# Kernel tuning notes

Hardware: AMD Instinct MI355X
Metric: run time of the kernel (lower is better)

The kernel has to match this reference:

```python
import jax, jax.numpy as jnp
import numpy as np

NUM_USERS = 200000
NUM_ITEMS = 100000
N_NODES = NUM_USERS + NUM_ITEMS
EMB_DIM = 64
NUM_LAYERS = 3
N_EDGES = 4800000


def setup_inputs() -> dict:
    key = jax.random.key(0)
    k1, k2, k3, k4, k5 = jax.random.split(key, 5)
    # Xavier-uniform-ish init scale for embeddings
    bound = float(np.sqrt(6.0 / (N_NODES + EMB_DIM)))
    user_emb = jax.random.uniform(k1, (NUM_USERS, EMB_DIM), jnp.float32, -bound, bound)
    item_emb = jax.random.uniform(k2, (NUM_ITEMS, EMB_DIM), jnp.float32, -bound, bound)
    adj_rows = jax.random.randint(k3, (N_EDGES,), 0, N_NODES, jnp.int32)
    adj_cols = jax.random.randint(k4, (N_EDGES,), 0, N_NODES, jnp.int32)
    # stand-in for symmetric-normalized adjacency values
    adj_vals = jax.random.uniform(k5, (N_EDGES,), jnp.float32) / 16.0
    return {"user_emb": user_emb, "item_emb": item_emb,
            "adj_rows": adj_rows, "adj_cols": adj_cols, "adj_vals": adj_vals}


def _spmm(rows, cols, vals, x):
    # y[r] = sum_{e: rows[e]==r} vals[e] * x[cols[e]]  -- COO SpMM
    gathered = x[cols] * vals[:, None]          # [E, D]
    return jax.ops.segment_sum(gathered, rows, num_segments=N_NODES)


def reference(user_emb, item_emb, adj_rows, adj_cols, adj_vals):
    emb = jnp.concatenate([user_emb, item_emb], axis=0)   # [N, D]
    acc = emb                                             # running sum over layers
    cur = emb
    for _ in range(NUM_LAYERS):
        cur = _spmm(adj_rows, adj_cols, adj_vals, cur)
        acc = acc + cur
    final = acc / jnp.asarray(NUM_LAYERS + 1, dtype=emb.dtype)
    return final[:NUM_USERS], final[NUM_USERS:]
```

## Files before the change

kernel.cpp:

```cpp
#include <hip/hip_runtime.h>
#include <hip/hip_fp16.h>


#define NU 200000
#define NI 100000
#define NN 300000
#define DD 64
#define NE 4800000
#define NB 512
#define RPB 586
#define NRPAD 640
#define CE_HIST 8192
#define CE_SCAT 6144
#define EPT (CE_SCAT / 1024)

#define FMA_MIX_LO(acc, h32, vv) \
    asm("v_fma_mix_f32 %0, %1, %2, %0 op_sel_hi:[1,0,0]" \
        : "+v"(acc) : "v"(h32), "v"(vv))
#define FMA_MIX_HI(acc, h32, vv) \
    asm("v_fma_mix_f32 %0, %1, %2, %0 op_sel:[1,0,0] op_sel_hi:[1,0,0]" \
        : "+v"(acc) : "v"(h32), "v"(vv))


__global__ void bucket_hist(const int* __restrict__ rows, int* __restrict__ bcnt) {
    __shared__ int h[NB];
    int tid = threadIdx.x;
    for (int i = tid; i < NB; i += 1024) h[i] = 0;
    __syncthreads();
    const int4* r4 = (const int4*)rows;
    int q0 = blockIdx.x * (CE_HIST / 4);
    for (int k = 0; k < CE_HIST / 4096; ++k) {
        int q = q0 + k * 1024 + tid;
        if (q < NE / 4) {
            int4 r = r4[q];
            atomicAdd(&h[(unsigned)r.x / RPB], 1);
            atomicAdd(&h[(unsigned)r.y / RPB], 1);
            atomicAdd(&h[(unsigned)r.z / RPB], 1);
            atomicAdd(&h[(unsigned)r.w / RPB], 1);
        }
    }
    __syncthreads();
    for (int i = tid; i < NB; i += 1024) {
        int c = h[i];
        if (c) atomicAdd(&bcnt[i], c);
    }
}


__global__ void bucket_scan(const int* __restrict__ bcnt, int* __restrict__ bbase,
                            int* __restrict__ gcursor) {
    __shared__ int sh[NB];
    int t = threadIdx.x;
    int v = bcnt[t];
    sh[t] = v;
    __syncthreads();
    for (int o = 1; o < NB; o <<= 1) {
        int x = (t >= o) ? sh[t - o] : 0;
        __syncthreads();
        sh[t] += x;
        __syncthreads();
    }
    int excl = sh[t] - v;
    bbase[t] = excl;
    gcursor[t] = excl;
    if (t == NB - 1) bbase[NB] = NE;
}


__global__ void bucket_scatter(const int* __restrict__ rows, const int* __restrict__ cols,
                               const float* __restrict__ vals,
                               int* __restrict__ gcursor, int2* __restrict__ recs) {
    __shared__ int  cnt[NB];
    __shared__ int  lofs[NB + 1];
    __shared__ int  dlt[NB];
    __shared__ int2 stg[CE_SCAT];
    int tid = threadIdx.x;
    if (tid < NB) cnt[tid] = 0;
    __syncthreads();
    int e0 = blockIdx.x * CE_SCAT;
    int r[EPT];
    #pragma unroll
    for (int k = 0; k < EPT; ++k) {
        int e = e0 + k * 1024 + tid;
        r[k] = -1;
        if (e < NE) {
            r[k] = rows[e];
            atomicAdd(&cnt[(unsigned)r[k] / RPB], 1);
        }
    }
    __syncthreads();
    if (tid < NB) lofs[tid] = cnt[tid];
    __syncthreads();
    for (int o = 1; o < NB; o <<= 1) {
        int x = 0;
        if (tid < NB && tid >= o) x = lofs[tid - o];
        __syncthreads();
        if (tid < NB) lofs[tid] += x;
        __syncthreads();
    }
    if (tid < NB) {
        int incl = lofs[tid];
        int c = cnt[tid];
        int excl = incl - c;
        int gb = c ? atomicAdd(&gcursor[tid], c) : 0;
        lofs[tid] = excl;
        dlt[tid] = gb - excl;
        cnt[tid] = 0;
        if (tid == NB - 1) lofs[NB] = incl;
    }
    __syncthreads();
    #pragma unroll
    for (int k = 0; k < EPT; ++k) {
        int e = e0 + k * 1024 + tid;
        if (e < NE) {
            int rr = r[k];
            int b = (unsigned)rr / RPB;
            int p = lofs[b] + atomicAdd(&cnt[b], 1);
            int rl = rr - b * RPB;
            stg[p] = make_int2((rl << 19) | cols[e], __float_as_int(vals[e]));
        }
    }
    __syncthreads();
    int total = lofs[NB];
    for (int i = tid; i < total; i += 1024) {
        int b = 0;
        #pragma unroll
        for (int s = NB >> 1; s > 0; s >>= 1)
            if (lofs[b + s] <= i) b += s;
        recs[dlt[b] + i] = stg[i];
    }
}


__global__ void fine_sort(const int* __restrict__ bbase, const int2* __restrict__ recs,
                          int2* __restrict__ edges, int* __restrict__ off) {
    __shared__ int cnt[NRPAD];
    __shared__ int scn[NRPAD];
    __shared__ int cur[NRPAD];
    int b = blockIdx.x, tid = threadIdx.x;
    int e0 = bbase[b], e1 = bbase[b + 1];
    if (tid < NRPAD) cnt[tid] = 0;
    __syncthreads();
    for (int e = e0 + tid; e < e1; e += 1024)
        atomicAdd(&cnt[recs[e].x >> 19], 1);
    __syncthreads();
    int v = 0;
    if (tid < NRPAD) { v = cnt[tid]; scn[tid] = v; }
    __syncthreads();
    for (int o = 1; o < NRPAD; o <<= 1) {
        int x = 0;
        if (tid < NRPAD && tid >= o) x = scn[tid - o];
        __syncthreads();
        if (tid < NRPAD) scn[tid] += x;
        __syncthreads();
    }
    if (tid < NRPAD) {
        int excl = e0 + scn[tid] - v;
        cur[tid] = excl;
        if (tid < RPB) {
            int row = b * RPB + tid;
            if (row < NN) off[row] = excl;
        }
    }
    if (b == 0 && tid == 0) off[NN] = NE;
    __syncthreads();
    for (int e = e0 + tid; e < e1; e += 1024) {
        int2 rc = recs[e];
        int rl = rc.x >> 19;
        int p = atomicAdd(&cur[rl], 1);
        edges[p] = make_int2(rc.x & 0x7FFFF, rc.y);
    }
}


__global__ void e_to_h(const float4* __restrict__ ue4, const float4* __restrict__ ie4,
                       uint2* __restrict__ h) {
    int i = blockIdx.x * blockDim.x + threadIdx.x;
    if (i >= NN * 16) return;
    float4 v = (i < NU * 16) ? ue4[i] : ie4[i - NU * 16];
    __half2 a = __float22half2_rn(make_float2(v.x, v.y));
    __half2 b = __float22half2_rn(make_float2(v.z, v.w));
    h[i] = make_uint2(*(unsigned*)&a, *(unsigned*)&b);
}


template <int MODE>
__global__ void spmm16_kernel(const int* __restrict__ off, const int2* __restrict__ edges,
                              const uint4* __restrict__ h8,
                              __half* __restrict__ nxtH,
                              float* __restrict__ acc,
                              const float* __restrict__ ue, const float* __restrict__ ie2) {
    int row  = (blockIdx.x * blockDim.x + threadIdx.x) >> 6;
    int lane = threadIdx.x & 63;
    int e    = lane >> 2;
    int d    = lane & 3;
    if (row >= NN) return;

    int start = off[row], end = off[row + 1];

    float s[16];
    #pragma unroll
    for (int k = 0; k < 16; ++k) s[k] = 0.f;

    for (int base = start; base < end; base += 16) {
        int ei = base + e;
        if (ei < end) {
            long long evl = __builtin_nontemporal_load((const long long*)&edges[ei]);
            int   c = (int)(unsigned)evl;
            float v = __int_as_float((int)(evl >> 32));
            const uint4* hp = &h8[(size_t)c * 8 + d * 2];
            uint4 ha = hp[0];
            uint4 hb = hp[1];
            FMA_MIX_LO(s[0],  ha.x, v); FMA_MIX_HI(s[1],  ha.x, v);
            FMA_MIX_LO(s[2],  ha.y, v); FMA_MIX_HI(s[3],  ha.y, v);
            FMA_MIX_LO(s[4],  ha.z, v); FMA_MIX_HI(s[5],  ha.z, v);
            FMA_MIX_LO(s[6],  ha.w, v); FMA_MIX_HI(s[7],  ha.w, v);
            FMA_MIX_LO(s[8],  hb.x, v); FMA_MIX_HI(s[9],  hb.x, v);
            FMA_MIX_LO(s[10], hb.y, v); FMA_MIX_HI(s[11], hb.y, v);
            FMA_MIX_LO(s[12], hb.z, v); FMA_MIX_HI(s[13], hb.z, v);
            FMA_MIX_LO(s[14], hb.w, v); FMA_MIX_HI(s[15], hb.w, v);
        }
    }

    {
        bool up = (lane & 4) != 0;
        #pragma unroll
        for (int k = 0; k < 8; ++k) {
            float keep = up ? s[k + 8] : s[k];
            float give = up ? s[k] : s[k + 8];
            s[k] = keep + __shfl_xor(give, 4);
        }
    }
    {
        bool up = (lane & 8) != 0;
        #pragma unroll
        for (int k = 0; k < 4; ++k) {
            float keep = up ? s[k + 4] : s[k];
            float give = up ? s[k] : s[k + 4];
            s[k] = keep + __shfl_xor(give, 8);
        }
    }
    {
        bool up = (lane & 16) != 0;
        #pragma unroll
        for (int k = 0; k < 2; ++k) {
            float keep = up ? s[k + 2] : s[k];
            float give = up ? s[k] : s[k + 2];
            s[k] = keep + __shfl_xor(give, 16);
        }
    }
    {
        bool up = (lane & 32) != 0;
        float keep = up ? s[1] : s[0];
        float give = up ? s[0] : s[1];
        s[0] = keep + __shfl_xor(give, 32);
    }

    int kstar = ((e & 1) << 3) | (((e >> 1) & 1) << 2) | (((e >> 2) & 1) << 1) | ((e >> 3) & 1);
    int idx = d * 16 + kstar;
    float val = s[0];
    size_t o = (size_t)row * DD + idx;

    if (MODE != 2) nxtH[o] = __float2half_rn(val);
    if (MODE == 0) {
        const float* p = (row < NU) ? ue : ie2;
        float e0 = __builtin_nontemporal_load(&p[o]);
        __builtin_nontemporal_store(e0 + val, &acc[o]);
    } else if (MODE == 1) {
        float a = __builtin_nontemporal_load(&acc[o]);
        __builtin_nontemporal_store(a + val, &acc[o]);
    } else {
        float a = __builtin_nontemporal_load(&acc[o]);
        __builtin_nontemporal_store((a + val) * 0.25f, &acc[o]);
    }
}


extern "C" void kernel_launch(void* const* d_in, const int* in_sizes, int n_in,
                              void* d_out, int out_size, void* d_ws, size_t ws_size,
                              hipStream_t stream) {
    const float* ue   = (const float*)d_in[0];
    const float* ie   = (const float*)d_in[1];
    const int*   rows = (const int*)d_in[2];
    const int*   cols = (const int*)d_in[3];
    const float* vals = (const float*)d_in[4];
    float* acc = (float*)d_out;

    char* ws = (char*)d_ws;
    size_t p = 0;
    auto alloc = [&](size_t bytes) -> void* {
        p = (p + 255) & ~(size_t)255;
        void* r = ws + p;
        p += bytes;
        return r;
    };
    int2*  edges   = (int2*) alloc((size_t)NE * 8);
    uint2* h0      = (uint2*)alloc((size_t)NN * 16 * 8);
    uint2* h1      = (uint2*)alloc((size_t)NN * 16 * 8);
    int*   bcnt    = (int*)  alloc((size_t)NB * 4);
    int*   bbase   = (int*)  alloc((size_t)(NB + 1) * 4);
    int*   gcursor = (int*)  alloc((size_t)NB * 4);
    int*   off     = (int*)  alloc((size_t)(NN + 1) * 4);
    int2*  recs = (int2*)h1;
    uint2* h2 = h0;

    hipMemsetAsync(bcnt, 0, (size_t)NB * 4, stream);
    bucket_hist   <<<(NE + CE_HIST - 1) / CE_HIST, 1024, 0, stream>>>(rows, bcnt);
    bucket_scan   <<<1, NB, 0, stream>>>(bcnt, bbase, gcursor);
    bucket_scatter<<<(NE + CE_SCAT - 1) / CE_SCAT, 1024, 0, stream>>>(rows, cols, vals, gcursor, recs);
    fine_sort     <<<NB, 1024, 0, stream>>>(bbase, recs, edges, off);

    const float* ie2 = ie - (size_t)NU * DD;
    e_to_h<<<(NN * 16 + 255) / 256, 256, 0, stream>>>(
        (const float4*)ue, (const float4*)ie2 + (size_t)NU * 16, h0);

    const int spmm_blocks = NN / 4;
    spmm16_kernel<0><<<spmm_blocks, 256, 0, stream>>>(off, edges, (const uint4*)h0, (__half*)h1, acc, ue, ie2);
    spmm16_kernel<1><<<spmm_blocks, 256, 0, stream>>>(off, edges, (const uint4*)h1, (__half*)h2, acc, ue, ie2);
    spmm16_kernel<2><<<spmm_blocks, 256, 0, stream>>>(off, edges, (const uint4*)h2, (__half*)h1, acc, ue, ie2);
}
```

Measured before the change: 668.7 us.

## Process two rows per wave in SpMM with edge prefetch and early acc loads

Remaps the SpMM so each 64-lane wave handles two rows with 32 lanes each, 8 edges per iteration instead of 16, which drops one shuffle reduction stage. Each lane now writes two adjacent outputs as a half2. The next edge record is software-prefetched, and the accumulator or base-embedding loads are issued before the loop to hide their latency. It also enlarges the histogram chunk per block. The aim is less idle-lane waste on rows with about 16 edges on average and better overlap of memory latency, at the cost of more loop iterations per row.

```diff
diff --git a/kernel.cpp b/kernel.cpp
--- a/kernel.cpp
+++ b/kernel.cpp
@@ -10,7 +10,7 @@
 #define NB 512
 #define RPB 586
 #define NRPAD 640
-#define CE_HIST 8192
+#define CE_HIST 32768
 #define CE_SCAT 6144
 #define EPT (CE_SCAT / 1024)
 
@@ -185,45 +185,74 @@
 
 
 template <int MODE>
-__global__ void spmm16_kernel(const int* __restrict__ off, const int2* __restrict__ edges,
+__global__ void spmm2r_kernel(const int* __restrict__ off, const int2* __restrict__ edges,
                               const uint4* __restrict__ h8,
                               __half* __restrict__ nxtH,
                               float* __restrict__ acc,
                               const float* __restrict__ ue, const float* __restrict__ ie2) {
-    int row  = (blockIdx.x * blockDim.x + threadIdx.x) >> 6;
+    int wave = (blockIdx.x * blockDim.x + threadIdx.x) >> 6;
     int lane = threadIdx.x & 63;
-    int e    = lane >> 2;
-    int d    = lane & 3;
-    if (row >= NN) return;
+    int l    = lane & 31;
+    int e    = l >> 2;
+    int d    = l & 3;
+    int row  = wave * 2 + (lane >> 5);
 
     int start = off[row], end = off[row + 1];
+
+    int idx = d * 16 + (((l >> 2) & 1) << 3) + (((l >> 3) & 1) << 2) + (((l >> 4) & 1) << 1);
+    size_t o = (size_t)row * DD + idx;
+
+    float b0, b1;
+    if (MODE == 0) {
+        const float* p = (row < NU) ? ue : ie2;
+        b0 = __builtin_nontemporal_load(&p[o]);
+        b1 = __builtin_nontemporal_load(&p[o + 1]);
+    } else {
+        b0 = __builtin_nontemporal_load(&acc[o]);
+        b1 = __builtin_nontemporal_load(&acc[o + 1]);
+    }
 
     float s[16];
     #pragma unroll
     for (int k = 0; k < 16; ++k) s[k] = 0.f;
 
-    for (int base = start; base < end; base += 16) {
-        int ei = base + e;
+    int ec = 0; float vc = 0.f;
+    {
+        int ei = start + e;
         if (ei < end) {
             long long evl = __builtin_nontemporal_load((const long long*)&edges[ei]);
-            int   c = (int)(unsigned)evl;
-            float v = __int_as_float((int)(evl >> 32));
-            const uint4* hp = &h8[(size_t)c * 8 + d * 2];
+            ec = (int)(unsigned)evl;
+            vc = __int_as_float((int)(evl >> 32));
+        }
+    }
+    for (int base = start; base < end; base += 8) {
+        int en = 0; float vn = 0.f;
+        {
+            int ein = base + 8 + e;
+            if (ein < end) {
+                long long evl = __builtin_nontemporal_load((const long long*)&edges[ein]);
+                en = (int)(unsigned)evl;
+                vn = __int_as_float((int)(evl >> 32));
+            }
+        }
+        if (base + e < end) {
+            const uint4* hp = &h8[(size_t)(unsigned)ec * 8 + d * 2];
             uint4 ha = hp[0];
             uint4 hb = hp[1];
-            FMA_MIX_LO(s[0],  ha.x, v); FMA_MIX_HI(s[1],  ha.x, v);
-            FMA_MIX_LO(s[2],  ha.y, v); FMA_MIX_HI(s[3],  ha.y, v);
-            FMA_MIX_LO(s[4],  ha.z, v); FMA_MIX_HI(s[5],  ha.z, v);
-            FMA_MIX_LO(s[6],  ha.w, v); FMA_MIX_HI(s[7],  ha.w, v);
-            FMA_MIX_LO(s[8],  hb.x, v); FMA_MIX_HI(s[9],  hb.x, v);
-            FMA_MIX_LO(s[10], hb.y, v); FMA_MIX_HI(s[11], hb.y, v);
-            FMA_MIX_LO(s[12], hb.z, v); FMA_MIX_HI(s[13], hb.z, v);
-            FMA_MIX_LO(s[14], hb.w, v); FMA_MIX_HI(s[15], hb.w, v);
-        }
+            FMA_MIX_LO(s[0],  ha.x, vc); FMA_MIX_HI(s[1],  ha.x, vc);
+            FMA_MIX_LO(s[2],  ha.y, vc); FMA_MIX_HI(s[3],  ha.y, vc);
+            FMA_MIX_LO(s[4],  ha.z, vc); FMA_MIX_HI(s[5],  ha.z, vc);
+            FMA_MIX_LO(s[6],  ha.w, vc); FMA_MIX_HI(s[7],  ha.w, vc);
+            FMA_MIX_LO(s[8],  hb.x, vc); FMA_MIX_HI(s[9],  hb.x, vc);
+            FMA_MIX_LO(s[10], hb.y, vc); FMA_MIX_HI(s[11], hb.y, vc);
+            FMA_MIX_LO(s[12], hb.z, vc); FMA_MIX_HI(s[13], hb.z, vc);
+            FMA_MIX_LO(s[14], hb.w, vc); FMA_MIX_HI(s[15], hb.w, vc);
+        }
+        ec = en; vc = vn;
     }
 
     {
-        bool up = (lane & 4) != 0;
+        bool up = (l & 4) != 0;
         #pragma unroll
         for (int k = 0; k < 8; ++k) {
             float keep = up ? s[k + 8] : s[k];
@@ -232,7 +261,7 @@
         }
     }
     {
-        bool up = (lane & 8) != 0;
+        bool up = (l & 8) != 0;
         #pragma unroll
         for (int k = 0; k < 4; ++k) {
             float keep = up ? s[k + 4] : s[k];
@@ -241,7 +270,7 @@
         }
     }
     {
-        bool up = (lane & 16) != 0;
+        bool up = (l & 16) != 0;
         #pragma unroll
         for (int k = 0; k < 2; ++k) {
             float keep = up ? s[k + 2] : s[k];
@@ -249,30 +278,15 @@
             s[k] = keep + __shfl_xor(give, 16);
         }
     }
-    {
-        bool up = (lane & 32) != 0;
-        float keep = up ? s[1] : s[0];
-        float give = up ? s[0] : s[1];
-        s[0] = keep + __shfl_xor(give, 32);
-    }
-
-    int kstar = ((e & 1) << 3) | (((e >> 1) & 1) << 2) | (((e >> 2) & 1) << 1) | ((e >> 3) & 1);
-    int idx = d * 16 + kstar;
-    float val = s[0];
-    size_t o = (size_t)row * DD + idx;
-
-    if (MODE != 2) nxtH[o] = __float2half_rn(val);
-    if (MODE == 0) {
-        const float* p = (row < NU) ? ue : ie2;
-        float e0 = __builtin_nontemporal_load(&p[o]);
-        __builtin_nontemporal_store(e0 + val, &acc[o]);
-    } else if (MODE == 1) {
-        float a = __builtin_nontemporal_load(&acc[o]);
-        __builtin_nontemporal_store(a + val, &acc[o]);
-    } else {
-        float a = __builtin_nontemporal_load(&acc[o]);
-        __builtin_nontemporal_store((a + val) * 0.25f, &acc[o]);
-    }
+
+    if (MODE != 2) {
+        __half2 hh = __float22half2_rn(make_float2(s[0], s[1]));
+        *(__half2*)&nxtH[o] = hh;
+    }
+    float r0 = b0 + s[0], r1 = b1 + s[1];
+    if (MODE == 2) { r0 *= 0.25f; r1 *= 0.25f; }
+    __builtin_nontemporal_store(r0, &acc[o]);
+    __builtin_nontemporal_store(r1, &acc[o + 1]);
 }
 
 
@@ -314,8 +328,8 @@
     e_to_h<<<(NN * 16 + 255) / 256, 256, 0, stream>>>(
         (const float4*)ue, (const float4*)ie2 + (size_t)NU * 16, h0);
 
-    const int spmm_blocks = NN / 4;
-    spmm16_kernel<0><<<spmm_blocks, 256, 0, stream>>>(off, edges, (const uint4*)h0, (__half*)h1, acc, ue, ie2);
-    spmm16_kernel<1><<<spmm_blocks, 256, 0, stream>>>(off, edges, (const uint4*)h1, (__half*)h2, acc, ue, ie2);
-    spmm16_kernel<2><<<spmm_blocks, 256, 0, stream>>>(off, edges, (const uint4*)h2, (__half*)h1, acc, ue, ie2);
-}
+    const int spmm_blocks = NN / 8;
+    spmm2r_kernel<0><<<spmm_blocks, 256, 0, stream>>>(off, edges, (const uint4*)h0, (__half*)h1, acc, ue, ie2);
+    spmm2r_kernel<1><<<spmm_blocks, 256, 0, stream>>>(off, edges, (const uint4*)h1, (__half*)h2, acc, ue, ie2);
+    spmm2r_kernel<2><<<spmm_blocks, 256, 0, stream>>>(off, edges, (const uint4*)h2, (__half*)h1, acc, ue, ie2);
+}
```

Measured after the change: 607.0 us. -9.2%, faster.
